# Performance work log

Measured on AMD Instinct MI355X. Metric: run time of the kernel, lower is better.

The kernel has to match this reference:

```python
import jax, jax.numpy as jnp
import numpy as np

B, T, D = 4, 2048, 1024
H = 16
HD = D // H  # 64
MAX_POS = 4096


def setup_inputs() -> dict:
    key = jax.random.key(0)
    k1, k2, k3, k4 = jax.random.split(key, 4)
    x = jax.random.normal(k1, (B, T, D), dtype=jnp.float32)
    position_ids = jnp.sort(jax.random.randint(k2, (B, T), 0, MAX_POS), axis=-1)
    Wqkv = jax.random.normal(k3, (D, 3 * D), dtype=jnp.float32) * (D ** -0.5)
    Wout = jax.random.normal(k4, (D, D), dtype=jnp.float32) * (D ** -0.5)
    return {"x": x, "position_ids": position_ids, "Wqkv": Wqkv, "Wout": Wout}


def reference(x, position_ids, Wqkv, Wout):
    Bv, Tv, Dv = x.shape
    # qkv projection: (B,T,3,H,HD)
    qkv = (x @ Wqkv).reshape(Bv, Tv, 3, H, HD)
    q, k, v = jnp.moveaxis(qkv, 2, 0)  # each (B,T,H,HD)
    q = q.transpose(0, 2, 1, 3)  # (B,H,T,HD)
    k = k.transpose(0, 2, 1, 3)
    v = v.transpose(0, 2, 1, 3)
    scale = 1.0 / jnp.sqrt(jnp.asarray(HD, dtype=x.dtype))
    attn = jnp.einsum('bhid,bhjd->bhij', q, k) * scale  # (B,H,T,T)
    # position-derived causal mask: attend only where pos_i >= pos_j
    causal_mask = position_ids[:, None, :, None] < position_ids[:, None, None, :]
    attn = jnp.where(causal_mask, -jnp.inf, attn)
    attn = jax.nn.softmax(attn, axis=-1)
    attn = jnp.nan_to_num(attn, nan=0.0)
    out = jnp.einsum('bhij,bhjd->bhid', attn, v)  # (B,H,T,HD)
    out = out.transpose(0, 2, 1, 3).reshape(Bv, Tv, Dv)
    return out @ Wout
```

## Files before the change

kernel.cpp:

```cpp
#include <hip/hip_runtime.h>
#include <math.h>

#define NB 4
#define NT 2048
#define ND 1024
#define NH 16
#define NHD 64
#define N3D 3072
#define M1 8192

typedef __attribute__((ext_vector_type(8))) short bf16x8;
typedef __attribute__((ext_vector_type(4))) float f32x4;
typedef __attribute__((ext_vector_type(16))) float f32x16;
typedef __attribute__((ext_vector_type(2))) int i32x2;
typedef unsigned short u16;
typedef unsigned int u32;

__device__ __forceinline__ u32 bf16rn(float f) {
    u32 u = __float_as_uint(f);
    return (u + 0x7FFFu + ((u >> 16) & 1u)) >> 16;
}
__device__ __forceinline__ u32 pack2(float a, float b) {
    return bf16rn(a) | (bf16rn(b) << 16);
}
__device__ __forceinline__ u32 cvtpk(float lo, float hi) {
    u32 r;
    asm("v_cvt_pk_bf16_f32 %0, %1, %2" : "=v"(r) : "v"(lo), "v"(hi));
    return r;
}
__device__ __forceinline__ void pswap(u32& a, u32& b) {
    i32x2 r = __builtin_amdgcn_permlane32_swap((int)a, (int)b, false, false);
    a = (u32)r.x; b = (u32)r.y;
}

__global__ __launch_bounds__(256) void convx_kernel(const float* __restrict__ in, u16* __restrict__ out) {
    const int idx = blockIdx.x * 256 + threadIdx.x;
    const float4 v = *reinterpret_cast<const float4*>(in + (size_t)idx * 4);
    *reinterpret_cast<uint2*>(out + (size_t)idx * 4) = make_uint2(pack2(v.x, v.y), pack2(v.z, v.w));
}

__global__ __launch_bounds__(256) void tconv_kernel(const float* __restrict__ in, u16* __restrict__ out,
                                                    int R, int C) {
    __shared__ float t[32][33];
    const int bx = blockIdx.x * 32, by = blockIdx.y * 32;
    const int x = threadIdx.x, y0 = threadIdx.y;
    #pragma unroll
    for (int yy = y0; yy < 32; yy += 8) t[yy][x] = in[(size_t)(by + yy) * C + bx + x];
    __syncthreads();
    #pragma unroll
    for (int yy = y0; yy < 32; yy += 8) out[(size_t)(bx + yy) * R + by + x] = (u16)bf16rn(t[x][yy]);
}

#define GEMM_PROLOGUE(Aptr, Btptr)                                                            \
    __shared__ __align__(16) u16 As[4096];                                                    \
    __shared__ __align__(16) u16 Bs[4096];                                                    \
    const int tid = threadIdx.x;                                                              \
    const int lane = tid & 63, wave = tid >> 6;                                               \
    const int wr = wave >> 1, wc = wave & 1;                                                  \
    const int n0 = blockIdx.x * 128, m0 = blockIdx.y * 128;                                   \
    const int c0 = tid, c1 = tid + 256;                                                       \
    const int pA0 = (c0 * 16) ^ ((((c0 * 16) >> 6) & 7) << 4);                                \
    const int pA1 = (c1 * 16) ^ ((((c1 * 16) >> 6) & 7) << 4);                                \
    const u16* gA0 = Aptr + (size_t)(m0 + (c0 >> 2)) * 1024 + (c0 & 3) * 8;                   \
    const u16* gA1 = Aptr + (size_t)(m0 + (c1 >> 2)) * 1024 + (c1 & 3) * 8;                   \
    const u16* gB0 = Btptr + (size_t)(n0 + (c0 >> 2)) * 1024 + (c0 & 3) * 8;                  \
    const u16* gB1 = Btptr + (size_t)(n0 + (c1 >> 2)) * 1024 + (c1 & 3) * 8;                  \
    int offA[4], offB[4];                                                                     \
    {                                                                                         \
        const int kb = (lane >> 4) * 16;                                                      \
        _Pragma("unroll")                                                                     \
        for (int mm = 0; mm < 4; ++mm) {                                                      \
            int row = wr * 64 + mm * 16 + (lane & 15);                                        \
            offA[mm] = (row * 64 + kb) ^ ((row & 7) << 4);                                    \
        }                                                                                     \
        _Pragma("unroll")                                                                     \
        for (int nn = 0; nn < 4; ++nn) {                                                      \
            int row = wc * 64 + nn * 16 + (lane & 15);                                        \
            offB[nn] = (row * 64 + kb) ^ ((row & 7) << 4);                                    \
        }                                                                                     \
    }                                                                                         \
    f32x4 acc[4][4];                                                                          \
    _Pragma("unroll")                                                                         \
    for (int mm = 0; mm < 4; ++mm)                                                            \
        _Pragma("unroll")                                                                     \
        for (int nn = 0; nn < 4; ++nn)                                                        \
            acc[mm][nn] = (f32x4){0.f, 0.f, 0.f, 0.f};                                        \
    uint4 va0 = *(const uint4*)gA0, va1 = *(const uint4*)gA1;                                 \
    uint4 vb0 = *(const uint4*)gB0, vb1 = *(const uint4*)gB1;                                 \
    for (int k0 = 0; k0 < 1024; k0 += 32) {                                                   \
        __syncthreads();                                                                      \
        *(uint4*)((char*)As + pA0) = va0;                                                     \
        *(uint4*)((char*)As + pA1) = va1;                                                     \
        *(uint4*)((char*)Bs + pA0) = vb0;                                                     \
        *(uint4*)((char*)Bs + pA1) = vb1;                                                     \
        __syncthreads();                                                                      \
        if (k0 + 32 < 1024) {                                                                 \
            gA0 += 32; gA1 += 32; gB0 += 32; gB1 += 32;                                       \
            va0 = *(const uint4*)gA0; va1 = *(const uint4*)gA1;                               \
            vb0 = *(const uint4*)gB0; vb1 = *(const uint4*)gB1;                               \
        }                                                                                     \
        bf16x8 aF[4], bF[4];                                                                  \
        _Pragma("unroll")                                                                     \
        for (int mm = 0; mm < 4; ++mm) aF[mm] = *(const bf16x8*)((const char*)As + offA[mm]); \
        _Pragma("unroll")                                                                     \
        for (int nn = 0; nn < 4; ++nn) bF[nn] = *(const bf16x8*)((const char*)Bs + offB[nn]); \
        _Pragma("unroll")                                                                     \
        for (int mm = 0; mm < 4; ++mm)                                                        \
            _Pragma("unroll")                                                                 \
            for (int nn = 0; nn < 4; ++nn)                                                    \
                acc[mm][nn] = __builtin_amdgcn_mfma_f32_16x16x32_bf16(bF[nn], aF[mm],         \
                                                                      acc[mm][nn], 0, 0, 0); \
    }

__global__ __launch_bounds__(256) void gemm_qkv_kernel(
    const u16* __restrict__ A, const u16* __restrict__ Bt,
    u16* __restrict__ Qo, u16* __restrict__ Ko, u16* __restrict__ Vo)
{
    GEMM_PROLOGUE(A, Bt)
    const float qsc = 0.18033688011112042f;
    const int col16 = lane & 15, g4 = (lane >> 4) << 2;
    const int nb0 = n0 + wc * 64;
    const int tb0 = m0 + wr * 64;
    const int s = nb0 >> 10;
    if (s == 0) {
        #pragma unroll
        for (int mm = 0; mm < 4; ++mm) {
            const int t = tb0 + mm * 16 + col16;
            const int bq = t >> 11, tt = t & 2047;
            #pragma unroll
            for (int nn = 0; nn < 4; ++nn) {
                const int n_abs = nb0 + nn * 16 + g4;
                const int hh = (n_abs >> 6) & 15, hd = n_abs & 63;
                uint2 w = make_uint2(pack2(acc[mm][nn][0] * qsc, acc[mm][nn][1] * qsc),
                                     pack2(acc[mm][nn][2] * qsc, acc[mm][nn][3] * qsc));
                *reinterpret_cast<uint2*>(&Qo[((size_t)((bq << 4) + hh) * 2048 + tt) * 64 + hd]) = w;
            }
        }
    } else if (s == 1) {
        #pragma unroll
        for (int mm = 0; mm < 4; ++mm) {
            const int t = tb0 + mm * 16 + col16;
            const int bq = t >> 11, tt = t & 2047;
            #pragma unroll
            for (int nn = 0; nn < 4; ++nn) {
                const int n_abs = nb0 + nn * 16 + g4;
                const int hh = (n_abs >> 6) & 15, hd = n_abs & 63;
                uint2 w = make_uint2(pack2(acc[mm][nn][0], acc[mm][nn][1]),
                                     pack2(acc[mm][nn][2], acc[mm][nn][3]));
                *reinterpret_cast<uint2*>(&Ko[((size_t)((bq << 4) + hh) * 2048 + tt) * 64 + hd]) = w;
            }
        }
    } else {
        #pragma unroll
        for (int mm = 0; mm < 4; ++mm) {
            const int t = tb0 + mm * 16 + col16;
            const int bq = t >> 11, tt = t & 2047;
            #pragma unroll
            for (int nn = 0; nn < 4; ++nn) {
                const int n_abs = nb0 + nn * 16 + g4;
                const int hh = (n_abs >> 6) & 15, hd = n_abs & 63;
                const size_t vbase = ((size_t)((bq << 4) + hh) * 64 + hd) * 2048 + tt;
                #pragma unroll
                for (int r = 0; r < 4; ++r)
                    Vo[vbase + (size_t)r * 2048] = (u16)bf16rn(acc[mm][nn][r]);
            }
        }
    }
}

__global__ __launch_bounds__(256) void gemm_out_kernel(
    const u16* __restrict__ A, const u16* __restrict__ Bt, float* __restrict__ C)
{
    GEMM_PROLOGUE(A, Bt)
    const int col16 = lane & 15, g4 = (lane >> 4) << 2;
    #pragma unroll
    for (int mm = 0; mm < 4; ++mm) {
        const int m = m0 + wr * 64 + mm * 16 + col16;
        #pragma unroll
        for (int nn = 0; nn < 4; ++nn) {
            const int n_a = n0 + wc * 64 + nn * 16 + g4;
            *reinterpret_cast<float4*>(&C[(size_t)m * 1024 + n_a]) =
                make_float4(acc[mm][nn][0], acc[mm][nn][1], acc[mm][nn][2], acc[mm][nn][3]);
        }
    }
}

__global__ __launch_bounds__(256) void attn4_kernel(
    const u16* __restrict__ Q, const u16* __restrict__ K, const u16* __restrict__ Vt,
    const int* __restrict__ pos, u16* __restrict__ AO)
{
    __shared__ int bndS[128];

    const int wg = ((blockIdx.x & 7) << 7) + (blockIdx.x >> 3);
    const int bh = wg >> 4;
    const int qb = 15 - (wg & 15);
    const int b = bh >> 4, h = bh & 15;
    const int tid = threadIdx.x, lane = tid & 63, wave = tid >> 6;
    const int col = lane & 31, hi = lane >> 5;

    if (tid < 128) {
        const int target = pos[b * 2048 + qb * 128 + tid];
        int lo = 0, hic = 2048;
        #pragma unroll
        for (int it = 0; it < 12; ++it) {
            const int mid = (lo + hic) >> 1;
            if (lo < hic) { if (pos[b * 2048 + mid] <= target) lo = mid + 1; else hic = mid; }
        }
        bndS[tid] = lo;
    }
    __syncthreads();

    const int bnd     = bndS[wave * 32 + col];
    const int bnd_min = bndS[wave * 32];
    const int bnd_max = bndS[wave * 32 + 31];

    const int i0 = qb * 128 + wave * 32;
    const size_t kvrow = (size_t)bh * 2048;
    const size_t vrow  = (size_t)bh * 64;

    bf16x8 qf[4];
    #pragma unroll
    for (int ds = 0; ds < 4; ++ds)
        qf[ds] = *(const bf16x8*)&Q[(kvrow + i0 + col) * 64 + ds * 16 + hi * 8];

    const int hi4 = 4 * hi;

    float mrun = -INFINITY, lrun = 0.f;
    f32x16 oT0, oT1;
    #pragma unroll
    for (int i = 0; i < 16; ++i) { oT0[i] = 0.f; oT1[i] = 0.f; }

    bf16x8 kf[4], vfa[2], vfb[2];
    #pragma unroll
    for (int ds = 0; ds < 4; ++ds)
        kf[ds] = *(const bf16x8*)&K[(kvrow + col) * 64 + ds * 16 + hi * 8];
    #pragma unroll
    for (int kh = 0; kh < 2; ++kh) {
        vfa[kh] = *(const bf16x8*)&Vt[(vrow + col) * 2048 + kh * 16 + hi * 8];
        vfb[kh] = *(const bf16x8*)&Vt[(vrow + 32 + col) * 2048 + kh * 16 + hi * 8];
    }

    for (int j0 = 0; j0 < bnd_max; j0 += 32) {
        f32x16 st;
        #pragma unroll
        for (int i = 0; i < 16; ++i) st[i] = 0.f;
        #pragma unroll
        for (int ds = 0; ds < 4; ++ds)
            st = __builtin_amdgcn_mfma_f32_32x32x16_bf16(kf[ds], qf[ds], st, 0, 0, 0);

        const int jn = (j0 + 32 < bnd_max) ? j0 + 32 : j0;
        bf16x8 kf2[4], vna[2], vnb[2];
        #pragma unroll
        for (int ds = 0; ds < 4; ++ds)
            kf2[ds] = *(const bf16x8*)&K[(kvrow + jn + col) * 64 + ds * 16 + hi * 8];
        #pragma unroll
        for (int kh = 0; kh < 2; ++kh) {
            vna[kh] = *(const bf16x8*)&Vt[(vrow + col) * 2048 + jn + kh * 16 + hi * 8];
            vnb[kh] = *(const bf16x8*)&Vt[(vrow + 32 + col) * 2048 + jn + kh * 16 + hi * 8];
        }

        if (j0 + 32 > bnd_min) {
            #pragma unroll
            for (int r = 0; r < 16; ++r) {
                const int kg = j0 + ((r & 3) + 8 * (r >> 2)) + hi4;
                if (kg >= bnd) st[r] = -INFINITY;
            }
        }

        float rm = st[0];
        #pragma unroll
        for (int r = 1; r < 16; ++r) rm = fmaxf(rm, st[r]);
        rm = fmaxf(rm, __shfl_xor(rm, 32));
        const float mnew = fmaxf(mrun, rm);
        const float factor = __builtin_amdgcn_exp2f(mrun - mnew);
        mrun = mnew;
        float psum = 0.f;
        #pragma unroll
        for (int r = 0; r < 16; ++r) {
            const float p = __builtin_amdgcn_exp2f(st[r] - mnew);
            st[r] = p;
            psum += p;
        }
        psum += __shfl_xor(psum, 32);
        lrun = lrun * factor + psum;
        #pragma unroll
        for (int i = 0; i < 16; ++i) { oT0[i] *= factor; oT1[i] *= factor; }

        u32 W[8];
        #pragma unroll
        for (int r = 0; r < 8; ++r) W[r] = cvtpk(st[2 * r], st[2 * r + 1]);

        u32 a0 = W[0], b0 = W[2]; pswap(a0, b0);
        u32 a1 = W[1], b1 = W[3]; pswap(a1, b1);
        u32 a2 = W[4], b2 = W[6]; pswap(a2, b2);
        u32 a3 = W[5], b3 = W[7]; pswap(a3, b3);
        union { u32 w[4]; bf16x8 v; } p0, p1;
        p0.w[0] = a0; p0.w[1] = a1; p0.w[2] = b0; p0.w[3] = b1;
        p1.w[0] = a2; p1.w[1] = a3; p1.w[2] = b2; p1.w[3] = b3;

        oT0 = __builtin_amdgcn_mfma_f32_32x32x16_bf16(vfa[0], p0.v, oT0, 0, 0, 0);
        oT0 = __builtin_amdgcn_mfma_f32_32x32x16_bf16(vfa[1], p1.v, oT0, 0, 0, 0);
        oT1 = __builtin_amdgcn_mfma_f32_32x32x16_bf16(vfb[0], p0.v, oT1, 0, 0, 0);
        oT1 = __builtin_amdgcn_mfma_f32_32x32x16_bf16(vfb[1], p1.v, oT1, 0, 0, 0);

        #pragma unroll
        for (int ds = 0; ds < 4; ++ds) kf[ds] = kf2[ds];
        #pragma unroll
        for (int kh = 0; kh < 2; ++kh) { vfa[kh] = vna[kh]; vfb[kh] = vnb[kh]; }
    }

    const float inv = 1.f / lrun;
    u16* dst = &AO[((size_t)(b * 2048 + i0 + col)) * 1024 + h * 64];
    #pragma unroll
    for (int w = 0; w < 8; ++w) {
        const int dloc = 8 * (w >> 1) + 2 * (w & 1) + hi4;
        *reinterpret_cast<u32*>(&dst[dloc])      = cvtpk(oT0[2 * w] * inv, oT0[2 * w + 1] * inv);
        *reinterpret_cast<u32*>(&dst[32 + dloc]) = cvtpk(oT1[2 * w] * inv, oT1[2 * w + 1] * inv);
    }
}

extern "C" void kernel_launch(void* const* d_in, const int* in_sizes, int n_in,
                              void* d_out, int out_size, void* d_ws, size_t ws_size,
                              hipStream_t stream) {
    (void)in_sizes; (void)n_in; (void)out_size; (void)ws_size;
    const float* x    = (const float*)d_in[0];
    const int*   pos  = (const int*)d_in[1];
    const float* Wqkv = (const float*)d_in[2];
    const float* Wout = (const float*)d_in[3];
    float* out = (float*)d_out;

    char* ws = (char*)d_ws;
    u16* xb    = (u16*)(ws);
    u16* WqkvT = (u16*)(ws + 16777216);
    u16* WoutT = (u16*)(ws + 23068672);
    u16* Qb    = (u16*)(ws + 25165824);
    u16* Kb    = (u16*)(ws + 41943040);
    u16* Vtb   = (u16*)(ws + 58720256);
    u16* AO    = xb;

    convx_kernel<<<dim3(M1 * ND / (256 * 4)), dim3(256), 0, stream>>>(x, xb);
    tconv_kernel<<<dim3(N3D / 32, ND / 32), dim3(32, 8), 0, stream>>>(Wqkv, WqkvT, ND, N3D);
    tconv_kernel<<<dim3(ND / 32, ND / 32), dim3(32, 8), 0, stream>>>(Wout, WoutT, ND, ND);
    gemm_qkv_kernel<<<dim3(N3D / 128, M1 / 128), dim3(256), 0, stream>>>(xb, WqkvT, Qb, Kb, Vtb);
    attn4_kernel<<<dim3(1024), dim3(256), 0, stream>>>(Qb, Kb, Vtb, pos, AO);
    gemm_out_kernel<<<dim3(ND / 128, M1 / 128), dim3(256), 0, stream>>>(AO, WoutT, out);
}
```

Before: 387.1 us.

## Split attention into single-wave blocks with lazy rescaling and no prefetch

```diff
diff --git a/kernel.cpp b/kernel.cpp
--- a/kernel.cpp
+++ b/kernel.cpp
@@ -58,7 +58,7 @@
     const int lane = tid & 63, wave = tid >> 6;                                               \
     const int wr = wave >> 1, wc = wave & 1;                                                  \
     const int n0 = blockIdx.x * 128, m0 = blockIdx.y * 128;                                   \
-    const int c0 = tid, c1 = tid + 256;                                                       \
+    const int c0 = tid, c1 = tid + 256;                                                      \
     const int pA0 = (c0 * 16) ^ ((((c0 * 16) >> 6) & 7) << 4);                                \
     const int pA1 = (c1 * 16) ^ ((((c1 * 16) >> 6) & 7) << 4);                                \
     const u16* gA0 = Aptr + (size_t)(m0 + (c0 >> 2)) * 1024 + (c0 & 3) * 8;                   \
@@ -185,36 +185,37 @@
     }
 }
 
-__global__ __launch_bounds__(256) void attn4_kernel(
+__global__ __launch_bounds__(64) void attn5_kernel(
     const u16* __restrict__ Q, const u16* __restrict__ K, const u16* __restrict__ Vt,
     const int* __restrict__ pos, u16* __restrict__ AO)
 {
-    __shared__ int bndS[128];
-
-    const int wg = ((blockIdx.x & 7) << 7) + (blockIdx.x >> 3);
-    const int bh = wg >> 4;
-    const int qb = 15 - (wg & 15);
+    const int bid = blockIdx.x;
+    const int wg  = ((bid & 7) << 9) + (bid >> 3);
+    const int bh  = wg >> 6;
+    const int qw  = 63 - (wg & 63);
     const int b = bh >> 4, h = bh & 15;
-    const int tid = threadIdx.x, lane = tid & 63, wave = tid >> 6;
+    const int lane = threadIdx.x;
     const int col = lane & 31, hi = lane >> 5;
-
-    if (tid < 128) {
-        const int target = pos[b * 2048 + qb * 128 + tid];
+    const int i0 = qw * 32;
+
+    int bnd;
+    {
+        const int target = pos[b * 2048 + i0 + col];
         int lo = 0, hic = 2048;
         #pragma unroll
         for (int it = 0; it < 12; ++it) {
             const int mid = (lo + hic) >> 1;
             if (lo < hic) { if (pos[b * 2048 + mid] <= target) lo = mid + 1; else hic = mid; }
         }
-        bndS[tid] = lo;
-    }
-    __syncthreads();
-
-    const int bnd     = bndS[wave * 32 + col];
-    const int bnd_min = bndS[wave * 32];
-    const int bnd_max = bndS[wave * 32 + 31];
-
-    const int i0 = qb * 128 + wave * 32;
+        bnd = lo;
+    }
+    int bmax = bnd, bmin = bnd;
+    #pragma unroll
+    for (int s = 1; s < 32; s <<= 1) {
+        bmax = max(bmax, __shfl_xor(bmax, s));
+        bmin = min(bmin, __shfl_xor(bmin, s));
+    }
+
     const size_t kvrow = (size_t)bh * 2048;
     const size_t vrow  = (size_t)bh * 64;
 
@@ -230,17 +231,17 @@
     #pragma unroll
     for (int i = 0; i < 16; ++i) { oT0[i] = 0.f; oT1[i] = 0.f; }
 
-    bf16x8 kf[4], vfa[2], vfb[2];
-    #pragma unroll
-    for (int ds = 0; ds < 4; ++ds)
-        kf[ds] = *(const bf16x8*)&K[(kvrow + col) * 64 + ds * 16 + hi * 8];
-    #pragma unroll
-    for (int kh = 0; kh < 2; ++kh) {
-        vfa[kh] = *(const bf16x8*)&Vt[(vrow + col) * 2048 + kh * 16 + hi * 8];
-        vfb[kh] = *(const bf16x8*)&Vt[(vrow + 32 + col) * 2048 + kh * 16 + hi * 8];
-    }
-
-    for (int j0 = 0; j0 < bnd_max; j0 += 32) {
+    for (int j0 = 0; j0 < bmax; j0 += 32) {
+        bf16x8 kf[4], vfa[2], vfb[2];
+        #pragma unroll
+        for (int ds = 0; ds < 4; ++ds)
+            kf[ds] = *(const bf16x8*)&K[(kvrow + j0 + col) * 64 + ds * 16 + hi * 8];
+        #pragma unroll
+        for (int kh = 0; kh < 2; ++kh) {
+            vfa[kh] = *(const bf16x8*)&Vt[(vrow + col) * 2048 + j0 + kh * 16 + hi * 8];
+            vfb[kh] = *(const bf16x8*)&Vt[(vrow + 32 + col) * 2048 + j0 + kh * 16 + hi * 8];
+        }
+
         f32x16 st;
         #pragma unroll
         for (int i = 0; i < 16; ++i) st[i] = 0.f;
@@ -248,18 +249,7 @@
         for (int ds = 0; ds < 4; ++ds)
             st = __builtin_amdgcn_mfma_f32_32x32x16_bf16(kf[ds], qf[ds], st, 0, 0, 0);
 
-        const int jn = (j0 + 32 < bnd_max) ? j0 + 32 : j0;
-        bf16x8 kf2[4], vna[2], vnb[2];
-        #pragma unroll
-        for (int ds = 0; ds < 4; ++ds)
-            kf2[ds] = *(const bf16x8*)&K[(kvrow + jn + col) * 64 + ds * 16 + hi * 8];
-        #pragma unroll
-        for (int kh = 0; kh < 2; ++kh) {
-            vna[kh] = *(const bf16x8*)&Vt[(vrow + col) * 2048 + jn + kh * 16 + hi * 8];
-            vnb[kh] = *(const bf16x8*)&Vt[(vrow + 32 + col) * 2048 + jn + kh * 16 + hi * 8];
-        }
-
-        if (j0 + 32 > bnd_min) {
+        if (j0 + 32 > bmin) {
             #pragma unroll
             for (int r = 0; r < 16; ++r) {
                 const int kg = j0 + ((r & 3) + 8 * (r >> 2)) + hi4;
@@ -271,20 +261,23 @@
         #pragma unroll
         for (int r = 1; r < 16; ++r) rm = fmaxf(rm, st[r]);
         rm = fmaxf(rm, __shfl_xor(rm, 32));
-        const float mnew = fmaxf(mrun, rm);
-        const float factor = __builtin_amdgcn_exp2f(mrun - mnew);
-        mrun = mnew;
+        if (__any(rm > mrun)) {
+            const float mnew = fmaxf(mrun, rm);
+            const float factor = __builtin_amdgcn_exp2f(mrun - mnew);
+            mrun = mnew;
+            lrun *= factor;
+            #pragma unroll
+            for (int i = 0; i < 16; ++i) { oT0[i] *= factor; oT1[i] *= factor; }
+        }
         float psum = 0.f;
         #pragma unroll
         for (int r = 0; r < 16; ++r) {
-            const float p = __builtin_amdgcn_exp2f(st[r] - mnew);
+            const float p = __builtin_amdgcn_exp2f(st[r] - mrun);
             st[r] = p;
             psum += p;
         }
         psum += __shfl_xor(psum, 32);
-        lrun = lrun * factor + psum;
-        #pragma unroll
-        for (int i = 0; i < 16; ++i) { oT0[i] *= factor; oT1[i] *= factor; }
+        lrun += psum;
 
         u32 W[8];
         #pragma unroll
@@ -302,11 +295,6 @@
         oT0 = __builtin_amdgcn_mfma_f32_32x32x16_bf16(vfa[1], p1.v, oT0, 0, 0, 0);
         oT1 = __builtin_amdgcn_mfma_f32_32x32x16_bf16(vfb[0], p0.v, oT1, 0, 0, 0);
         oT1 = __builtin_amdgcn_mfma_f32_32x32x16_bf16(vfb[1], p1.v, oT1, 0, 0, 0);
-
-        #pragma unroll
-        for (int ds = 0; ds < 4; ++ds) kf[ds] = kf2[ds];
-        #pragma unroll
-        for (int kh = 0; kh < 2; ++kh) { vfa[kh] = vna[kh]; vfb[kh] = vnb[kh]; }
     }
 
     const float inv = 1.f / lrun;
@@ -342,6 +330,6 @@
     tconv_kernel<<<dim3(N3D / 32, ND / 32), dim3(32, 8), 0, stream>>>(Wqkv, WqkvT, ND, N3D);
     tconv_kernel<<<dim3(ND / 32, ND / 32), dim3(32, 8), 0, stream>>>(Wout, WoutT, ND, ND);
     gemm_qkv_kernel<<<dim3(N3D / 128, M1 / 128), dim3(256), 0, stream>>>(xb, WqkvT, Qb, Kb, Vtb);
-    attn4_kernel<<<dim3(1024), dim3(256), 0, stream>>>(Qb, Kb, Vtb, pos, AO);
+    attn5_kernel<<<dim3(4096), dim3(64), 0, stream>>>(Qb, Kb, Vtb, pos, AO);
     gemm_out_kernel<<<dim3(ND / 128, M1 / 128), dim3(256), 0, stream>>>(AO, WoutT, out);
 }
```

Result: faster. 356.6 us (-7.9%).
